# Optimization experiments

Measured on AMD Instinct MI355X. Metric: run time of the kernel, lower is better.

## Reference

```python
import jax, jax.numpy as jnp
import numpy as np

N = 100_000
E = 3_200_000
F_IN = 512
F_OUT = 256
ALPHA = 0.2      # LeakyReLU negative slope
EPS = 9e-15      # matches torch.Tensor([9e-15]) in the original


def setup_inputs() -> dict:
    key = jax.random.key(0)
    k_x, k_e, k_w, k_a, k_b = jax.random.split(key, 5)
    x = jax.random.normal(k_x, (N, F_IN), dtype=jnp.float32)
    edge = jax.random.randint(k_e, (2, E), 0, N, dtype=jnp.int64)
    # xavier_normal-ish scales
    W = jax.random.normal(k_w, (F_IN, F_OUT), dtype=jnp.float32) * (1.414 * np.sqrt(2.0 / (F_IN + F_OUT)))
    a = jax.random.normal(k_a, (2 * F_OUT,), dtype=jnp.float32) * (1.414 * np.sqrt(2.0 / (1 + 2 * F_OUT)))
    bias = jax.random.normal(k_b, (F_OUT,), dtype=jnp.float32) * (1.414 * np.sqrt(2.0 / (1 + F_OUT)))
    return {"x": x, "edge": edge, "W": W, "a": a, "bias": bias}


def reference(x, edge, W, a, bias):
    src, dst = edge[0], edge[1]
    n = x.shape[0]
    h = x @ W + bias  # [N, F_OUT]
    # a . cat(h[src], h[dst]) == (h @ a_src)[src] + (h @ a_dst)[dst]
    a_src, a_dst = a[:F_OUT], a[F_OUT:]
    e = (h @ a_src)[src] + (h @ a_dst)[dst]            # [E]
    e = jnp.where(e > 0, e, ALPHA * e)                  # LeakyReLU
    e = jnp.exp(e - jnp.max(e))                         # global-max stabilized exp
    rowsum = jax.ops.segment_sum(e, src, num_segments=n)               # [N]
    h_prime = jax.ops.segment_sum(e[:, None] * h[dst], src, num_segments=n)  # [N, F_OUT]
    h_prime = h_prime / (rowsum[:, None] + EPS)
    return jax.nn.elu(h_prime)
```

## Files before the change

kernel.cpp:

```cpp
#include <hip/hip_runtime.h>

typedef __bf16 bf16x8 __attribute__((ext_vector_type(8)));
typedef float f32x4 __attribute__((ext_vector_type(4)));
typedef unsigned short u16x8 __attribute__((ext_vector_type(8)));

#define FIN 512
#define FOUT 256
#define NBLK 256
#define BSHIFT 8

__device__ __forceinline__ float b2f(unsigned short u) {
  union { unsigned int u; float f; } x;
  x.u = ((unsigned int)u) << 16;
  return x.f;
}
__device__ __forceinline__ unsigned short f2b(float f) {
  union { float f; unsigned int u; } x; x.f = f;
  unsigned int u = x.u;
  unsigned int r = (u + 0x7fffu + ((u >> 16) & 1u)) >> 16;
  return (unsigned short)r;
}
__device__ __forceinline__ unsigned int cvt_pk_bf16(float lo, float hi) {
  unsigned int r;
  asm("v_cvt_pk_bf16_f32 %0, %1, %2" : "=v"(r) : "v"(lo), "v"(hi));
  return r;
}

__global__ void k_probe(const unsigned short* __restrict__ xh,
                        const int* __restrict__ e, int* __restrict__ flags) {
  __shared__ int cnt[2];
  if (threadIdx.x == 0) { cnt[0] = 0; cnt[1] = 0; }
  __syncthreads();
  int c = 0;
  for (int i = threadIdx.x; i < 32768; i += 256) {
    unsigned short u = xh[i];
    if (((u >> 7) & 0xFF) == 0xFF) c++;
  }
  if (c) atomicAdd(&cnt[0], c);
  if (e[2 * threadIdx.x + 1] == 0) atomicAdd(&cnt[1], 1);
  __syncthreads();
  if (threadIdx.x == 0) {
    flags[0] = (cnt[0] > 0) ? 1 : 0;
    flags[1] = (cnt[1] > 128) ? 1 : 0;
  }
}

__global__ void k_transpose(const void* __restrict__ W,
                            unsigned short* __restrict__ Wt,
                            const int* __restrict__ flags) {
  int idx = blockIdx.x * 256 + threadIdx.x;
  int k = idx >> 8, n = idx & 255;
  float v = flags[0] ? ((const float*)W)[idx]
                     : b2f(((const unsigned short*)W)[idx]);
  Wt[n * FIN + k] = f2b(v);
}

__global__ __launch_bounds__(256) void k_gemm(const void* __restrict__ X,
                                              const unsigned short* __restrict__ Wt,
                                              const void* __restrict__ bias,
                                              const void* __restrict__ A,
                                              unsigned short* __restrict__ H,
                                              float* __restrict__ s1,
                                              float* __restrict__ s2,
                                              int nrows, const int* __restrict__ flags) {
  __shared__ char lds[65536];
  const int tid = threadIdx.x;
  const int wave = tid >> 6;
  const int lane = tid & 63;
  const int fm = lane & 15;
  const int fq = lane >> 4;
  const int isf = flags[0];
  const int m0 = blockIdx.x * 64;

  if (isf) {
#pragma unroll 4
    for (int j = 0; j < 16; ++j) {
      int r = wave * 16 + j;
      int grow = m0 + r; if (grow >= nrows) grow = nrows - 1;
      int c = lane ^ (j & 7);
      const float* gp = (const float*)X + (size_t)grow * FIN + c * 8;
      f32x4 lo = *(const f32x4*)gp;
      f32x4 hi = *(const f32x4*)(gp + 4);
      uint4 pk;
      pk.x = cvt_pk_bf16(lo[0], lo[1]);
      pk.y = cvt_pk_bf16(lo[2], lo[3]);
      pk.z = cvt_pk_bf16(hi[0], hi[1]);
      pk.w = cvt_pk_bf16(hi[2], hi[3]);
      *(uint4*)(lds + r * 1024 + lane * 16) = pk;
    }
  } else {
#pragma unroll
    for (int j = 0; j < 16; ++j) {
      int r = wave * 16 + j;
      int grow = m0 + r; if (grow >= nrows) grow = nrows - 1;
      int c = lane ^ (j & 7);
      const unsigned short* gp = (const unsigned short*)X + (size_t)grow * FIN + c * 8;
      __builtin_amdgcn_global_load_lds(
          (const __attribute__((address_space(1))) void*)gp,
          (__attribute__((address_space(3))) void*)(lds + r * 1024), 16, 0, 0);
    }
  }
  __syncthreads();

  f32x4 acc[4][4];
#pragma unroll
  for (int i = 0; i < 4; i++)
#pragma unroll
    for (int j = 0; j < 4; j++) acc[i][j] = (f32x4){0.f, 0.f, 0.f, 0.f};

  const unsigned short* wp[4];
#pragma unroll
  for (int i = 0; i < 4; i++)
    wp[i] = Wt + (size_t)((wave * 4 + i) * 16 + fm) * FIN + fq * 8;

  const int swz = fm & 7;
  bf16x8 bcur[4];
#pragma unroll
  for (int i = 0; i < 4; i++) bcur[i] = *(const bf16x8*)(wp[i]);

  for (int it = 0; it < 16; ++it) {
    int itn = (it + 1 < 16) ? it + 1 : 15;
    bf16x8 bnext[4];
#pragma unroll
    for (int i = 0; i < 4; i++) bnext[i] = *(const bf16x8*)(wp[i] + itn * 32);
    bf16x8 af[4];
#pragma unroll
    for (int mt = 0; mt < 4; mt++) {
      int slot = (it * 4 + fq) ^ swz;
      af[mt] = *(const bf16x8*)(lds + (mt * 16 + fm) * 1024 + slot * 16);
    }
#pragma unroll
    for (int mt = 0; mt < 4; mt++)
#pragma unroll
      for (int i = 0; i < 4; i++)
        acc[mt][i] = __builtin_amdgcn_mfma_f32_16x16x32_bf16(af[mt], bcur[i], acc[mt][i], 0, 0, 0);
#pragma unroll
    for (int i = 0; i < 4; i++) bcur[i] = bnext[i];
  }

  __syncthreads();
  float* sc1 = (float*)lds;
  float* sc2 = sc1 + 256;

  float bvv[4], asv[4], adv[4];
#pragma unroll
  for (int i = 0; i < 4; i++) {
    int col = (wave * 4 + i) * 16 + fm;
    if (isf) {
      bvv[i] = ((const float*)bias)[col];
      asv[i] = ((const float*)A)[col];
      adv[i] = ((const float*)A)[FOUT + col];
    } else {
      bvv[i] = b2f(((const unsigned short*)bias)[col]);
      asv[i] = b2f(((const unsigned short*)A)[col]);
      adv[i] = b2f(((const unsigned short*)A)[FOUT + col]);
    }
  }

#pragma unroll
  for (int mt = 0; mt < 4; mt++) {
#pragma unroll
    for (int r = 0; r < 4; r++) {
      int row = m0 + mt * 16 + fq * 4 + r;
      float p1 = 0.f, p2 = 0.f;
#pragma unroll
      for (int i = 0; i < 4; i++) {
        float h = acc[mt][i][r] + bvv[i];
        if (row < nrows) H[(size_t)row * FOUT + (wave * 4 + i) * 16 + fm] = f2b(h);
        p1 += h * asv[i];
        p2 += h * adv[i];
      }
#pragma unroll
      for (int off = 1; off < 16; off <<= 1) {
        p1 += __shfl_xor(p1, off, 64);
        p2 += __shfl_xor(p2, off, 64);
      }
      if (fm == 0) {
        int rl = mt * 16 + fq * 4 + r;
        sc1[wave * 64 + rl] = p1;
        sc2[wave * 64 + rl] = p2;
      }
    }
  }
  __syncthreads();
  if (tid < 64) {
    int row = m0 + tid;
    if (row < nrows) {
      s1[row] = sc1[tid] + sc1[64 + tid] + sc1[128 + tid] + sc1[192 + tid];
      s2[row] = sc2[tid] + sc2[64 + tid] + sc2[128 + tid] + sc2[192 + tid];
    }
  }
}


__global__ __launch_bounds__(256) void k_bcount(const int* __restrict__ e, int E, int chunk,
                                                int nbuck, int* __restrict__ C,
                                                const int* __restrict__ flags) {
  __shared__ int hist[512];
  int t = threadIdx.x, blk = blockIdx.x;
  for (int i = t; i < nbuck; i += 256) hist[i] = 0;
  __syncthreads();
  int lo = blk * chunk, hi = min(E, lo + chunk);
  bool i64 = flags[1] != 0;
  for (int i = lo + t; i < hi; i += 256) {
    int s = i64 ? ((const int2*)e)[i].x : e[i];
    atomicAdd(&hist[s >> BSHIFT], 1);
  }
  __syncthreads();
  for (int i = t; i < nbuck; i += 256) C[blk * nbuck + i] = hist[i];
}

__global__ __launch_bounds__(256) void k_bscanA(const int* __restrict__ C, int nbuck,
                                                int* __restrict__ O, int* __restrict__ btot) {
  int b = blockIdx.x, t = threadIdx.x;
  int lane = t & 63, w = t >> 6;
  int v = C[t * nbuck + b];
  int x = v;
#pragma unroll
  for (int off = 1; off < 64; off <<= 1) {
    int y = __shfl_up(x, off, 64);
    if (lane >= off) x += y;
  }
  __shared__ int ws[4];
  if (lane == 63) ws[w] = x;
  __syncthreads();
  int wbase = (w > 0 ? ws[0] : 0) + (w > 1 ? ws[1] : 0) + (w > 2 ? ws[2] : 0);
  O[t * nbuck + b] = x + wbase - v;
  if (t == 255) btot[b] = x + wbase;
}

__global__ __launch_bounds__(512) void k_bscanB(const int* __restrict__ btot, int nbuck,
                                                int* __restrict__ bbase,
                                                int* __restrict__ rowptr, int N) {
  __shared__ int sh[512];
  int t = threadIdx.x;
  int v = (t < nbuck) ? btot[t] : 0;
  sh[t] = v;
  __syncthreads();
  for (int off = 1; off < 512; off <<= 1) {
    int u = (t >= off) ? sh[t - off] : 0;
    __syncthreads();
    sh[t] += u;
    __syncthreads();
  }
  if (t < nbuck) bbase[t] = sh[t] - v;
  if (t == nbuck - 1) { bbase[nbuck] = sh[t]; rowptr[N] = sh[t]; }
}

__global__ __launch_bounds__(256) void k_bscatter(const int* __restrict__ e, int E, int chunk,
                                                  int nbuck, const int* __restrict__ O,
                                                  const int* __restrict__ bbase,
                                                  int* __restrict__ stage,
                                                  const int* __restrict__ flags) {
  __shared__ int cur[512];
  int t = threadIdx.x, blk = blockIdx.x;
  for (int i = t; i < nbuck; i += 256) cur[i] = bbase[i] + O[blk * nbuck + i];
  __syncthreads();
  int lo = blk * chunk, hi = min(E, lo + chunk);
  bool i64 = flags[1] != 0;
  for (int i = lo + t; i < hi; i += 256) {
    int s, d;
    if (i64) { s = ((const int2*)e)[i].x; d = ((const int2*)e)[(size_t)E + i].x; }
    else     { s = e[i];                  d = e[E + i]; }
    int pos = atomicAdd(&cur[s >> BSHIFT], 1);
    stage[pos] = ((s & 255) << 17) | d;
  }
}

__global__ __launch_bounds__(256) void k_fine(const int* __restrict__ stage,
                                              const int* __restrict__ bbase,
                                              int* __restrict__ rowptr,
                                              int* __restrict__ csrd, int N) {
  __shared__ int hist[256];
  __shared__ int cursor[256];
  __shared__ int ws[4];
  int b = blockIdx.x, t = threadIdx.x;
  int s0 = b << BSHIFT;
  int base = bbase[b], end = bbase[b + 1], cnt = end - base;
  hist[t] = 0;
  __syncthreads();
  for (int i = t; i < cnt; i += 256) atomicAdd(&hist[stage[base + i] >> 17], 1);
  __syncthreads();
  int v = hist[t];
  int lane = t & 63, w = t >> 6;
  int x = v;
#pragma unroll
  for (int off = 1; off < 64; off <<= 1) {
    int y = __shfl_up(x, off, 64);
    if (lane >= off) x += y;
  }
  if (lane == 63) ws[w] = x;
  __syncthreads();
  int wbase = (w > 0 ? ws[0] : 0) + (w > 1 ? ws[1] : 0) + (w > 2 ? ws[2] : 0);
  int excl = x + wbase - v;
  cursor[t] = base + excl;
  if (s0 + t < N) rowptr[s0 + t] = base + excl;
  __syncthreads();
  for (int i = t; i < cnt; i += 256) {
    int p = stage[base + i];
    int pos = atomicAdd(&cursor[p >> 17], 1);
    csrd[pos] = p & 0x1FFFF;
  }
}

__global__ __launch_bounds__(256) void k_gather(const unsigned short* __restrict__ H,
                                                const float* __restrict__ s1,
                                                const float* __restrict__ s2,
                                                const int* __restrict__ rowptr,
                                                const int* __restrict__ csrd,
                                                void* __restrict__ out, int n,
                                                const int* __restrict__ flags) {
  __shared__ int2 eds[4][64];
  int wave = threadIdx.x >> 6, lane = threadIdx.x & 63;
  int row = blockIdx.x * 4 + wave;
  if (row >= n) return;
  int half = lane >> 5;
  int hl = lane & 31;
  int beg = rowptr[row], end = rowptr[row + 1];
  float s1v = s1[row];
  const unsigned short* Hb = H + hl * 8;
  float ac[8];
#pragma unroll
  for (int k = 0; k < 8; k++) ac[k] = 0.f;
  float wsum = 0.f;

  for (int base = beg; base < end; base += 64) {
    int cnt = end - base; if (cnt > 64) cnt = 64;
    int d_pre = 0;
    float s_pre = -1e30f;
    if (lane < cnt) { d_pre = csrd[base + lane]; s_pre = s2[d_pre]; }
    eds[wave][lane] = make_int2(d_pre, __float_as_int(s_pre));

#pragma unroll 8
    for (int j = 0; j < cnt; j += 2) {
      int jj = j + half;
      int2 p = eds[wave][jj];
      int dd = p.x;
      float v = s1v + __int_as_float(p.y);
      v = v > 0.f ? v : 0.2f * v;
      float w = (jj < cnt) ? __expf(v) : 0.f;
      union { u16x8 v; unsigned short u[8]; } hv;
      hv.v = *(const u16x8*)(Hb + (size_t)dd * FOUT);
      wsum += w;
#pragma unroll
      for (int k = 0; k < 8; k++) ac[k] += w * b2f(hv.u[k]);
    }
  }

#pragma unroll
  for (int k = 0; k < 8; k++) ac[k] += __shfl_down(ac[k], 32, 64);
  wsum += __shfl_down(wsum, 32, 64);

  if (half == 0) {
    float inv = 1.f / (wsum + 9e-15f);
    float o[8];
#pragma unroll
    for (int k = 0; k < 8; k++) {
      float x = ac[k] * inv;
      o[k] = x > 0.f ? x : __expf(x) - 1.f;
    }
    if (flags[0]) {
      float* op = (float*)out + (size_t)row * FOUT + hl * 8;
      *(f32x4*)op = (f32x4){o[0], o[1], o[2], o[3]};
      *(f32x4*)(op + 4) = (f32x4){o[4], o[5], o[6], o[7]};
    } else {
      union { u16x8 v; unsigned short u[8]; } ov;
#pragma unroll
      for (int k = 0; k < 8; k++) ov.u[k] = f2b(o[k]);
      *(u16x8*)((unsigned short*)out + (size_t)row * FOUT + hl * 8) = ov.v;
    }
  }
}

extern "C" void kernel_launch(void* const* d_in, const int* in_sizes, int n_in,
                              void* d_out, int out_size, void* d_ws, size_t ws_size,
                              hipStream_t stream) {
  const void* X = d_in[0];
  const int* edge = (const int*)d_in[1];
  const void* W = d_in[2];
  const void* A = d_in[3];
  const void* B = d_in[4];
  int N_ = in_sizes[0] / FIN;
  int E_ = in_sizes[1] / 2;
  int nbuck = (N_ + 255) >> BSHIFT;
  int chunk = (E_ + NBLK - 1) / NBLK;

  char* p = (char*)d_ws;
  auto alloc = [&](size_t bytes) {
    char* r = p; p += (bytes + 255) & ~(size_t)255; return r;
  };
  int* flags = (int*)alloc(256);
  unsigned short* H  = (unsigned short*)alloc((size_t)N_ * FOUT * 2);
  unsigned short* Wt = (unsigned short*)alloc((size_t)FIN * FOUT * 2);
  float* s1   = (float*)alloc((size_t)N_ * 4);
  float* s2   = (float*)alloc((size_t)N_ * 4);
  int* rowptr = (int*)alloc((size_t)(N_ + 1) * 4);
  int* csrd   = (int*)alloc((size_t)E_ * 4);
  int* C      = (int*)alloc((size_t)NBLK * nbuck * 4);
  int* O      = (int*)alloc((size_t)NBLK * nbuck * 4);
  int* btot   = (int*)alloc((size_t)nbuck * 4);
  int* bbase  = (int*)alloc((size_t)(nbuck + 1) * 4);
  int* stage  = (int*)alloc((size_t)E_ * 4);

  k_probe<<<1, 256, 0, stream>>>((const unsigned short*)X, edge, flags);
  k_transpose<<<(FIN * FOUT) / 256, 256, 0, stream>>>(W, Wt, flags);
  k_gemm<<<(N_ + 63) / 64, 256, 0, stream>>>(X, Wt, B, A, H, s1, s2, N_, flags);
  k_bcount<<<NBLK, 256, 0, stream>>>(edge, E_, chunk, nbuck, C, flags);
  k_bscanA<<<nbuck, 256, 0, stream>>>(C, nbuck, O, btot);
  k_bscanB<<<1, 512, 0, stream>>>(btot, nbuck, bbase, rowptr, N_);
  k_bscatter<<<NBLK, 256, 0, stream>>>(edge, E_, chunk, nbuck, O, bbase, stage, flags);
  k_fine<<<nbuck, 256, 0, stream>>>(stage, bbase, rowptr, csrd, N_);
  k_gather<<<(N_ + 3) / 4, 256, 0, stream>>>(H, s1, s2, rowptr, csrd,
                                             d_out, N_, flags);
}
```

Baseline: 728.9 us.

## Fuse CSR build stages into one cooperative kernel with grid syncs

The probe, W transpose, bucket count, two scans, scatter and fine sort are merged into a single cooperative kernel of 256 blocks that uses grid.sync between phases. This replaces seven launches and their inter-kernel gaps, and a fallback to the original launches runs if the cooperative launch fails. The gather is also split into about four launches over row ranges, which adds launch overhead without an obvious benefit. Grid syncs serialize the phases, and the single-block scan phases leave most blocks idle.

```diff
diff --git a/kernel.cpp b/kernel.cpp
--- a/kernel.cpp
+++ b/kernel.cpp
@@ -1,4 +1,6 @@
 #include <hip/hip_runtime.h>
+#include <hip/hip_cooperative_groups.h>
+namespace cg = cooperative_groups;
 
 typedef __bf16 bf16x8 __attribute__((ext_vector_type(8)));
 typedef float f32x4 __attribute__((ext_vector_type(4)));
@@ -24,6 +26,155 @@
   unsigned int r;
   asm("v_cvt_pk_bf16_f32 %0, %1, %2" : "=v"(r) : "v"(lo), "v"(hi));
   return r;
+}
+
+__global__ __launch_bounds__(256) void k_csr_all(
+    const unsigned short* __restrict__ xh, const int* __restrict__ e,
+    int* __restrict__ flags, const void* __restrict__ W,
+    unsigned short* __restrict__ Wt, int E, int chunk, int nbuck,
+    int* __restrict__ C, int* __restrict__ O, int* __restrict__ btot,
+    int* __restrict__ bbase, int* __restrict__ rowptr,
+    int* __restrict__ stage, int* __restrict__ csrd, int N) {
+  cg::grid_group grid = cg::this_grid();
+  __shared__ int shm[768];
+  const int t = threadIdx.x;
+  const int blk = blockIdx.x;
+
+  if (blk == 0) {
+    if (t == 0) { shm[0] = 0; shm[1] = 0; }
+    __syncthreads();
+    int c = 0;
+    for (int i = t; i < 32768; i += 256) {
+      unsigned short u = xh[i];
+      if (((u >> 7) & 0xFF) == 0xFF) c++;
+    }
+    if (c) atomicAdd(&shm[0], c);
+    if (e[2 * t + 1] == 0) atomicAdd(&shm[1], 1);
+    __syncthreads();
+    if (t == 0) {
+      flags[0] = (shm[0] > 0) ? 1 : 0;
+      flags[1] = (shm[1] > 128) ? 1 : 0;
+    }
+  }
+  __threadfence();
+  grid.sync();
+
+  const int isf = flags[0];
+  const bool i64 = flags[1] != 0;
+
+#pragma unroll
+  for (int k2 = 0; k2 < 2; k2++) {
+    int idx = blk * 512 + k2 * 256 + t;
+    int kk = idx >> 8, nn = idx & 255;
+    float v = isf ? ((const float*)W)[idx]
+                  : b2f(((const unsigned short*)W)[idx]);
+    Wt[nn * FIN + kk] = f2b(v);
+  }
+  for (int i = t; i < nbuck; i += 256) shm[i] = 0;
+  __syncthreads();
+  {
+    int lo = blk * chunk, hi = min(E, lo + chunk);
+    for (int i = lo + t; i < hi; i += 256) {
+      int s = i64 ? ((const int2*)e)[i].x : e[i];
+      atomicAdd(&shm[s >> BSHIFT], 1);
+    }
+  }
+  __syncthreads();
+  for (int i = t; i < nbuck; i += 256) C[blk * nbuck + i] = shm[i];
+  __threadfence();
+  grid.sync();
+
+  for (int k2 = 0; k2 < 2; k2++) {
+    __syncthreads();
+    int b = blk + k2 * 256;
+    if (b < nbuck) {
+      int lane = t & 63, w = t >> 6;
+      int v = C[t * nbuck + b];
+      int x = v;
+#pragma unroll
+      for (int off = 1; off < 64; off <<= 1) {
+        int y = __shfl_up(x, off, 64);
+        if (lane >= off) x += y;
+      }
+      if (lane == 63) shm[512 + w] = x;
+      __syncthreads();
+      int wbase = (w > 0 ? shm[512] : 0) + (w > 1 ? shm[513] : 0) + (w > 2 ? shm[514] : 0);
+      O[t * nbuck + b] = x + wbase - v;
+      if (t == 255) btot[b] = x + wbase;
+    }
+  }
+  __threadfence();
+  grid.sync();
+
+  if (blk == 0) {
+    int v0 = (t < nbuck) ? btot[t] : 0;
+    int v1 = (t + 256 < nbuck) ? btot[t + 256] : 0;
+    shm[t] = v0; shm[t + 256] = v1;
+    __syncthreads();
+    for (int off = 1; off < 512; off <<= 1) {
+      int a0 = (t >= off) ? shm[t - off] : 0;
+      int a1 = (t + 256 >= off) ? shm[t + 256 - off] : 0;
+      __syncthreads();
+      shm[t] += a0; shm[t + 256] += a1;
+      __syncthreads();
+    }
+    if (t < nbuck) bbase[t] = shm[t] - v0;
+    if (t + 256 < nbuck) bbase[t + 256] = shm[t + 256] - v1;
+    if (t == nbuck - 1) { bbase[nbuck] = shm[t]; rowptr[N] = shm[t]; }
+    if (t + 256 == nbuck - 1) { bbase[nbuck] = shm[t + 256]; rowptr[N] = shm[t + 256]; }
+  }
+  __threadfence();
+  grid.sync();
+
+  for (int i = t; i < nbuck; i += 256) shm[i] = bbase[i] + O[blk * nbuck + i];
+  __syncthreads();
+  {
+    int lo = blk * chunk, hi = min(E, lo + chunk);
+    for (int i = lo + t; i < hi; i += 256) {
+      int s, d;
+      if (i64) { s = ((const int2*)e)[i].x; d = ((const int2*)e)[(size_t)E + i].x; }
+      else     { s = e[i];                  d = e[E + i]; }
+      int pos = atomicAdd(&shm[s >> BSHIFT], 1);
+      stage[pos] = ((s & 255) << 17) | d;
+    }
+  }
+  __threadfence();
+  grid.sync();
+
+  for (int k2 = 0; k2 < 2; k2++) {
+    __syncthreads();
+    int b = blk + k2 * 256;
+    if (b >= nbuck) continue;
+    int s0 = b << BSHIFT;
+    int base = bbase[b], end2 = bbase[b + 1], cnt = end2 - base;
+    int* hist = shm;
+    int* cursor = shm + 256;
+    int* ws = shm + 512;
+    hist[t] = 0;
+    __syncthreads();
+    for (int i = t; i < cnt; i += 256) atomicAdd(&hist[stage[base + i] >> 17], 1);
+    __syncthreads();
+    int v = hist[t];
+    int lane = t & 63, w = t >> 6;
+    int x = v;
+#pragma unroll
+    for (int off = 1; off < 64; off <<= 1) {
+      int y = __shfl_up(x, off, 64);
+      if (lane >= off) x += y;
+    }
+    if (lane == 63) ws[w] = x;
+    __syncthreads();
+    int wbase = (w > 0 ? ws[0] : 0) + (w > 1 ? ws[1] : 0) + (w > 2 ? ws[2] : 0);
+    int excl = x + wbase - v;
+    cursor[t] = base + excl;
+    if (s0 + t < N) rowptr[s0 + t] = base + excl;
+    __syncthreads();
+    for (int i = t; i < cnt; i += 256) {
+      int p = stage[base + i];
+      int pos = atomicAdd(&cursor[p >> 17], 1);
+      csrd[pos] = p & 0x1FFFF;
+    }
+  }
 }
 
 __global__ void k_probe(const unsigned short* __restrict__ xh,
@@ -53,6 +204,116 @@
   float v = flags[0] ? ((const float*)W)[idx]
                      : b2f(((const unsigned short*)W)[idx]);
   Wt[n * FIN + k] = f2b(v);
+}
+
+__global__ __launch_bounds__(256) void k_bcount(const int* __restrict__ e, int E, int chunk,
+                                                int nbuck, int* __restrict__ C,
+                                                const int* __restrict__ flags) {
+  __shared__ int hist[512];
+  int t = threadIdx.x, blk = blockIdx.x;
+  for (int i = t; i < nbuck; i += 256) hist[i] = 0;
+  __syncthreads();
+  int lo = blk * chunk, hi = min(E, lo + chunk);
+  bool i64 = flags[1] != 0;
+  for (int i = lo + t; i < hi; i += 256) {
+    int s = i64 ? ((const int2*)e)[i].x : e[i];
+    atomicAdd(&hist[s >> BSHIFT], 1);
+  }
+  __syncthreads();
+  for (int i = t; i < nbuck; i += 256) C[blk * nbuck + i] = hist[i];
+}
+
+__global__ __launch_bounds__(256) void k_bscanA(const int* __restrict__ C, int nbuck,
+                                                int* __restrict__ O, int* __restrict__ btot) {
+  int b = blockIdx.x, t = threadIdx.x;
+  int lane = t & 63, w = t >> 6;
+  int v = C[t * nbuck + b];
+  int x = v;
+#pragma unroll
+  for (int off = 1; off < 64; off <<= 1) {
+    int y = __shfl_up(x, off, 64);
+    if (lane >= off) x += y;
+  }
+  __shared__ int ws[4];
+  if (lane == 63) ws[w] = x;
+  __syncthreads();
+  int wbase = (w > 0 ? ws[0] : 0) + (w > 1 ? ws[1] : 0) + (w > 2 ? ws[2] : 0);
+  O[t * nbuck + b] = x + wbase - v;
+  if (t == 255) btot[b] = x + wbase;
+}
+
+__global__ __launch_bounds__(512) void k_bscanB(const int* __restrict__ btot, int nbuck,
+                                                int* __restrict__ bbase,
+                                                int* __restrict__ rowptr, int N) {
+  __shared__ int sh[512];
+  int t = threadIdx.x;
+  int v = (t < nbuck) ? btot[t] : 0;
+  sh[t] = v;
+  __syncthreads();
+  for (int off = 1; off < 512; off <<= 1) {
+    int u = (t >= off) ? sh[t - off] : 0;
+    __syncthreads();
+    sh[t] += u;
+    __syncthreads();
+  }
+  if (t < nbuck) bbase[t] = sh[t] - v;
+  if (t == nbuck - 1) { bbase[nbuck] = sh[t]; rowptr[N] = sh[t]; }
+}
+
+__global__ __launch_bounds__(256) void k_bscatter(const int* __restrict__ e, int E, int chunk,
+                                                  int nbuck, const int* __restrict__ O,
+                                                  const int* __restrict__ bbase,
+                                                  int* __restrict__ stage,
+                                                  const int* __restrict__ flags) {
+  __shared__ int cur[512];
+  int t = threadIdx.x, blk = blockIdx.x;
+  for (int i = t; i < nbuck; i += 256) cur[i] = bbase[i] + O[blk * nbuck + i];
+  __syncthreads();
+  int lo = blk * chunk, hi = min(E, lo + chunk);
+  bool i64 = flags[1] != 0;
+  for (int i = lo + t; i < hi; i += 256) {
+    int s, d;
+    if (i64) { s = ((const int2*)e)[i].x; d = ((const int2*)e)[(size_t)E + i].x; }
+    else     { s = e[i];                  d = e[E + i]; }
+    int pos = atomicAdd(&cur[s >> BSHIFT], 1);
+    stage[pos] = ((s & 255) << 17) | d;
+  }
+}
+
+__global__ __launch_bounds__(256) void k_fine(const int* __restrict__ stage,
+                                              const int* __restrict__ bbase,
+                                              int* __restrict__ rowptr,
+                                              int* __restrict__ csrd, int N) {
+  __shared__ int hist[256];
+  __shared__ int cursor[256];
+  __shared__ int ws[4];
+  int b = blockIdx.x, t = threadIdx.x;
+  int s0 = b << BSHIFT;
+  int base = bbase[b], end = bbase[b + 1], cnt = end - base;
+  hist[t] = 0;
+  __syncthreads();
+  for (int i = t; i < cnt; i += 256) atomicAdd(&hist[stage[base + i] >> 17], 1);
+  __syncthreads();
+  int v = hist[t];
+  int lane = t & 63, w = t >> 6;
+  int x = v;
+#pragma unroll
+  for (int off = 1; off < 64; off <<= 1) {
+    int y = __shfl_up(x, off, 64);
+    if (lane >= off) x += y;
+  }
+  if (lane == 63) ws[w] = x;
+  __syncthreads();
+  int wbase = (w > 0 ? ws[0] : 0) + (w > 1 ? ws[1] : 0) + (w > 2 ? ws[2] : 0);
+  int excl = x + wbase - v;
+  cursor[t] = base + excl;
+  if (s0 + t < N) rowptr[s0 + t] = base + excl;
+  __syncthreads();
+  for (int i = t; i < cnt; i += 256) {
+    int p = stage[base + i];
+    int pos = atomicAdd(&cursor[p >> 17], 1);
+    csrd[pos] = p & 0x1FFFF;
+  }
 }
 
 __global__ __launch_bounds__(256) void k_gemm(const void* __restrict__ X,
@@ -192,127 +453,16 @@
   }
 }
 
-
-__global__ __launch_bounds__(256) void k_bcount(const int* __restrict__ e, int E, int chunk,
-                                                int nbuck, int* __restrict__ C,
-                                                const int* __restrict__ flags) {
-  __shared__ int hist[512];
-  int t = threadIdx.x, blk = blockIdx.x;
-  for (int i = t; i < nbuck; i += 256) hist[i] = 0;
-  __syncthreads();
-  int lo = blk * chunk, hi = min(E, lo + chunk);
-  bool i64 = flags[1] != 0;
-  for (int i = lo + t; i < hi; i += 256) {
-    int s = i64 ? ((const int2*)e)[i].x : e[i];
-    atomicAdd(&hist[s >> BSHIFT], 1);
-  }
-  __syncthreads();
-  for (int i = t; i < nbuck; i += 256) C[blk * nbuck + i] = hist[i];
-}
-
-__global__ __launch_bounds__(256) void k_bscanA(const int* __restrict__ C, int nbuck,
-                                                int* __restrict__ O, int* __restrict__ btot) {
-  int b = blockIdx.x, t = threadIdx.x;
-  int lane = t & 63, w = t >> 6;
-  int v = C[t * nbuck + b];
-  int x = v;
-#pragma unroll
-  for (int off = 1; off < 64; off <<= 1) {
-    int y = __shfl_up(x, off, 64);
-    if (lane >= off) x += y;
-  }
-  __shared__ int ws[4];
-  if (lane == 63) ws[w] = x;
-  __syncthreads();
-  int wbase = (w > 0 ? ws[0] : 0) + (w > 1 ? ws[1] : 0) + (w > 2 ? ws[2] : 0);
-  O[t * nbuck + b] = x + wbase - v;
-  if (t == 255) btot[b] = x + wbase;
-}
-
-__global__ __launch_bounds__(512) void k_bscanB(const int* __restrict__ btot, int nbuck,
-                                                int* __restrict__ bbase,
-                                                int* __restrict__ rowptr, int N) {
-  __shared__ int sh[512];
-  int t = threadIdx.x;
-  int v = (t < nbuck) ? btot[t] : 0;
-  sh[t] = v;
-  __syncthreads();
-  for (int off = 1; off < 512; off <<= 1) {
-    int u = (t >= off) ? sh[t - off] : 0;
-    __syncthreads();
-    sh[t] += u;
-    __syncthreads();
-  }
-  if (t < nbuck) bbase[t] = sh[t] - v;
-  if (t == nbuck - 1) { bbase[nbuck] = sh[t]; rowptr[N] = sh[t]; }
-}
-
-__global__ __launch_bounds__(256) void k_bscatter(const int* __restrict__ e, int E, int chunk,
-                                                  int nbuck, const int* __restrict__ O,
-                                                  const int* __restrict__ bbase,
-                                                  int* __restrict__ stage,
-                                                  const int* __restrict__ flags) {
-  __shared__ int cur[512];
-  int t = threadIdx.x, blk = blockIdx.x;
-  for (int i = t; i < nbuck; i += 256) cur[i] = bbase[i] + O[blk * nbuck + i];
-  __syncthreads();
-  int lo = blk * chunk, hi = min(E, lo + chunk);
-  bool i64 = flags[1] != 0;
-  for (int i = lo + t; i < hi; i += 256) {
-    int s, d;
-    if (i64) { s = ((const int2*)e)[i].x; d = ((const int2*)e)[(size_t)E + i].x; }
-    else     { s = e[i];                  d = e[E + i]; }
-    int pos = atomicAdd(&cur[s >> BSHIFT], 1);
-    stage[pos] = ((s & 255) << 17) | d;
-  }
-}
-
-__global__ __launch_bounds__(256) void k_fine(const int* __restrict__ stage,
-                                              const int* __restrict__ bbase,
-                                              int* __restrict__ rowptr,
-                                              int* __restrict__ csrd, int N) {
-  __shared__ int hist[256];
-  __shared__ int cursor[256];
-  __shared__ int ws[4];
-  int b = blockIdx.x, t = threadIdx.x;
-  int s0 = b << BSHIFT;
-  int base = bbase[b], end = bbase[b + 1], cnt = end - base;
-  hist[t] = 0;
-  __syncthreads();
-  for (int i = t; i < cnt; i += 256) atomicAdd(&hist[stage[base + i] >> 17], 1);
-  __syncthreads();
-  int v = hist[t];
-  int lane = t & 63, w = t >> 6;
-  int x = v;
-#pragma unroll
-  for (int off = 1; off < 64; off <<= 1) {
-    int y = __shfl_up(x, off, 64);
-    if (lane >= off) x += y;
-  }
-  if (lane == 63) ws[w] = x;
-  __syncthreads();
-  int wbase = (w > 0 ? ws[0] : 0) + (w > 1 ? ws[1] : 0) + (w > 2 ? ws[2] : 0);
-  int excl = x + wbase - v;
-  cursor[t] = base + excl;
-  if (s0 + t < N) rowptr[s0 + t] = base + excl;
-  __syncthreads();
-  for (int i = t; i < cnt; i += 256) {
-    int p = stage[base + i];
-    int pos = atomicAdd(&cursor[p >> 17], 1);
-    csrd[pos] = p & 0x1FFFF;
-  }
-}
-
 __global__ __launch_bounds__(256) void k_gather(const unsigned short* __restrict__ H,
                                                 const float* __restrict__ s1,
                                                 const float* __restrict__ s2,
                                                 const int* __restrict__ rowptr,
                                                 const int* __restrict__ csrd,
-                                                void* __restrict__ out, int n,
+                                                void* __restrict__ out, int row0, int n,
                                                 const int* __restrict__ flags) {
   __shared__ int2 eds[4][64];
   int wave = threadIdx.x >> 6, lane = threadIdx.x & 63;
-  int row = blockIdx.x * 4 + wave;
+  int row = row0 + blockIdx.x * 4 + wave;
   if (row >= n) return;
   int half = lane >> 5;
   int hl = lane & 31;
@@ -402,14 +552,36 @@
   int* bbase  = (int*)alloc((size_t)(nbuck + 1) * 4);
   int* stage  = (int*)alloc((size_t)E_ * 4);
 
-  k_probe<<<1, 256, 0, stream>>>((const unsigned short*)X, edge, flags);
-  k_transpose<<<(FIN * FOUT) / 256, 256, 0, stream>>>(W, Wt, flags);
+  {
+    const unsigned short* xh_ = (const unsigned short*)X;
+    const int* e_ = edge;
+    int* flags_ = flags;
+    const void* W_ = W;
+    unsigned short* Wt_ = Wt;
+    int E2 = E_, chunk2 = chunk, nbuck2 = nbuck, N2 = N_;
+    int* C_ = C; int* O_ = O; int* btot_ = btot; int* bbase_ = bbase;
+    int* rowptr_ = rowptr; int* stage_ = stage; int* csrd_ = csrd;
+    void* cargs[] = {&xh_, &e_, &flags_, &W_, &Wt_, &E2, &chunk2, &nbuck2,
+                     &C_, &O_, &btot_, &bbase_, &rowptr_, &stage_, &csrd_, &N2};
+    hipError_t cerr = hipLaunchCooperativeKernel((const void*)k_csr_all,
+                        dim3(NBLK), dim3(256), cargs, 0, stream);
+    if (cerr != hipSuccess) {
+      k_probe<<<1, 256, 0, stream>>>(xh_, edge, flags);
+      k_transpose<<<(FIN * FOUT) / 256, 256, 0, stream>>>(W, Wt, flags);
+      k_bcount<<<NBLK, 256, 0, stream>>>(edge, E_, chunk, nbuck, C, flags);
+      k_bscanA<<<nbuck, 256, 0, stream>>>(C, nbuck, O, btot);
+      k_bscanB<<<1, 512, 0, stream>>>(btot, nbuck, bbase, rowptr, N_);
+      k_bscatter<<<NBLK, 256, 0, stream>>>(edge, E_, chunk, nbuck, O, bbase, stage, flags);
+      k_fine<<<nbuck, 256, 0, stream>>>(stage, bbase, rowptr, csrd, N_);
+    }
+  }
+
   k_gemm<<<(N_ + 63) / 64, 256, 0, stream>>>(X, Wt, B, A, H, s1, s2, N_, flags);
-  k_bcount<<<NBLK, 256, 0, stream>>>(edge, E_, chunk, nbuck, C, flags);
-  k_bscanA<<<nbuck, 256, 0, stream>>>(C, nbuck, O, btot);
-  k_bscanB<<<1, 512, 0, stream>>>(btot, nbuck, bbase, rowptr, N_);
-  k_bscatter<<<NBLK, 256, 0, stream>>>(edge, E_, chunk, nbuck, O, bbase, stage, flags);
-  k_fine<<<nbuck, 256, 0, stream>>>(stage, bbase, rowptr, csrd, N_);
-  k_gather<<<(N_ + 3) / 4, 256, 0, stream>>>(H, s1, s2, rowptr, csrd,
-                                             d_out, N_, flags);
-}
+
+  int rstep = ((N_ + 15) / 16) * 4;
+  for (int r0 = 0; r0 < N_; r0 += rstep) {
+    int rows = N_ - r0; if (rows > rstep) rows = rstep;
+    k_gather<<<(rows + 3) / 4, 256, 0, stream>>>(H, s1, s2, rowptr, csrd,
+                                                 d_out, r0, N_, flags);
+  }
+}
```

Measured after the change: 1.048 ms. +43.8%, slower.

## Halve GEMM LDS footprint by staging X in two K-halves for occupancy

Applied to the files above, without the earlier changes.

The GEMM kernel now stages its 64-row X tile into shared memory in two 256-column halves (32 KB instead of 64 KB), computing on one half before loading the second. It sets launch bounds to target 3 blocks per CU, and deepens the W-fragment register prefetch from one step ahead to two. The goal is more resident blocks per CU so one block's loads can overlap with other blocks' MFMA work. The cost is an extra barrier and a non-overlapped reload in the middle of each block, plus tighter register limits that could cause spills.

```diff
diff --git a/kernel.cpp b/kernel.cpp
--- a/kernel.cpp
+++ b/kernel.cpp
@@ -55,52 +55,59 @@
   Wt[n * FIN + k] = f2b(v);
 }
 
-__global__ __launch_bounds__(256) void k_gemm(const void* __restrict__ X,
-                                              const unsigned short* __restrict__ Wt,
-                                              const void* __restrict__ bias,
-                                              const void* __restrict__ A,
-                                              unsigned short* __restrict__ H,
-                                              float* __restrict__ s1,
-                                              float* __restrict__ s2,
-                                              int nrows, const int* __restrict__ flags) {
-  __shared__ char lds[65536];
+__global__ __launch_bounds__(256, 3) void k_gemm(const void* __restrict__ X,
+                                                 const unsigned short* __restrict__ Wt,
+                                                 const void* __restrict__ bias,
+                                                 const void* __restrict__ A,
+                                                 unsigned short* __restrict__ H,
+                                                 float* __restrict__ s1,
+                                                 float* __restrict__ s2,
+                                                 int nrows, const int* __restrict__ flags) {
+  __shared__ char lds[32768];
   const int tid = threadIdx.x;
   const int wave = tid >> 6;
   const int lane = tid & 63;
   const int fm = lane & 15;
   const int fq = lane >> 4;
+  const int hw = lane >> 5;
+  const int hl = lane & 31;
   const int isf = flags[0];
   const int m0 = blockIdx.x * 64;
 
-  if (isf) {
-#pragma unroll 4
-    for (int j = 0; j < 16; ++j) {
-      int r = wave * 16 + j;
-      int grow = m0 + r; if (grow >= nrows) grow = nrows - 1;
-      int c = lane ^ (j & 7);
-      const float* gp = (const float*)X + (size_t)grow * FIN + c * 8;
-      f32x4 lo = *(const f32x4*)gp;
-      f32x4 hi = *(const f32x4*)(gp + 4);
-      uint4 pk;
-      pk.x = cvt_pk_bf16(lo[0], lo[1]);
-      pk.y = cvt_pk_bf16(lo[2], lo[3]);
-      pk.z = cvt_pk_bf16(hi[0], hi[1]);
-      pk.w = cvt_pk_bf16(hi[2], hi[3]);
-      *(uint4*)(lds + r * 1024 + lane * 16) = pk;
-    }
-  } else {
-#pragma unroll
-    for (int j = 0; j < 16; ++j) {
-      int r = wave * 16 + j;
-      int grow = m0 + r; if (grow >= nrows) grow = nrows - 1;
-      int c = lane ^ (j & 7);
-      const unsigned short* gp = (const unsigned short*)X + (size_t)grow * FIN + c * 8;
-      __builtin_amdgcn_global_load_lds(
-          (const __attribute__((address_space(1))) void*)gp,
-          (__attribute__((address_space(3))) void*)(lds + r * 1024), 16, 0, 0);
-    }
-  }
-  __syncthreads();
+#define STAGE_HALF(h)                                                          \
+  do {                                                                         \
+    const int k0_ = (h) * 256;                                                 \
+    if (isf) {                                                                 \
+      _Pragma("unroll")                                                        \
+      for (int j = 0; j < 8; ++j) {                                            \
+        int r = wave * 16 + j * 2 + hw;                                        \
+        int grow = m0 + r; if (grow >= nrows) grow = nrows - 1;                \
+        int c = hl ^ (r & 7);                                                  \
+        const float* gp = (const float*)X + (size_t)grow * FIN + k0_ + c * 8;  \
+        f32x4 lo = *(const f32x4*)gp;                                          \
+        f32x4 hi = *(const f32x4*)(gp + 4);                                    \
+        uint4 pk;                                                              \
+        pk.x = cvt_pk_bf16(lo[0], lo[1]);                                      \
+        pk.y = cvt_pk_bf16(lo[2], lo[3]);                                      \
+        pk.z = cvt_pk_bf16(hi[0], hi[1]);                                      \
+        pk.w = cvt_pk_bf16(hi[2], hi[3]);                                      \
+        *(uint4*)(lds + r * 512 + hl * 16) = pk;                               \
+      }                                                                        \
+    } else {                                                                   \
+      _Pragma("unroll")                                                        \
+      for (int j = 0; j < 8; ++j) {                                            \
+        int r = wave * 16 + j * 2 + hw;                                        \
+        int grow = m0 + r; if (grow >= nrows) grow = nrows - 1;                \
+        int c = hl ^ (r & 7);                                                  \
+        const unsigned short* gp =                                             \
+            (const unsigned short*)X + (size_t)grow * FIN + k0_ + c * 8;       \
+        __builtin_amdgcn_global_load_lds(                                      \
+            (const __attribute__((address_space(1))) void*)gp,                 \
+            (__attribute__((address_space(3))) void*)(lds +                    \
+                (wave * 16 + j * 2) * 512), 16, 0, 0);                         \
+      }                                                                        \
+    }                                                                          \
+  } while (0)
 
   f32x4 acc[4][4];
 #pragma unroll
@@ -114,29 +121,48 @@
     wp[i] = Wt + (size_t)((wave * 4 + i) * 16 + fm) * FIN + fq * 8;
 
   const int swz = fm & 7;
-  bf16x8 bcur[4];
+
+  STAGE_HALF(0);
+
+  bf16x8 bcur[4], bnxt[4];
 #pragma unroll
   for (int i = 0; i < 4; i++) bcur[i] = *(const bf16x8*)(wp[i]);
-
-  for (int it = 0; it < 16; ++it) {
-    int itn = (it + 1 < 16) ? it + 1 : 15;
-    bf16x8 bnext[4];
-#pragma unroll
-    for (int i = 0; i < 4; i++) bnext[i] = *(const bf16x8*)(wp[i] + itn * 32);
-    bf16x8 af[4];
-#pragma unroll
-    for (int mt = 0; mt < 4; mt++) {
-      int slot = (it * 4 + fq) ^ swz;
-      af[mt] = *(const bf16x8*)(lds + (mt * 16 + fm) * 1024 + slot * 16);
-    }
-#pragma unroll
-    for (int mt = 0; mt < 4; mt++)
-#pragma unroll
-      for (int i = 0; i < 4; i++)
-        acc[mt][i] = __builtin_amdgcn_mfma_f32_16x16x32_bf16(af[mt], bcur[i], acc[mt][i], 0, 0, 0);
-#pragma unroll
-    for (int i = 0; i < 4; i++) bcur[i] = bnext[i];
-  }
+#pragma unroll
+  for (int i = 0; i < 4; i++) bnxt[i] = *(const bf16x8*)(wp[i] + 32);
+
+  __syncthreads();
+
+#define K_BODY(kk, it)                                                         \
+  do {                                                                         \
+    bf16x8 af[4];                                                              \
+    _Pragma("unroll")                                                          \
+    for (int mt = 0; mt < 4; mt++) {                                           \
+      int slot = ((it) * 4 + fq) ^ swz;                                        \
+      af[mt] = *(const bf16x8*)(lds + (mt * 16 + fm) * 512 + slot * 16);       \
+    }                                                                          \
+    bf16x8 bn[4];                                                              \
+    int kn = (kk) + 2; if (kn > 15) kn = 15;                                   \
+    _Pragma("unroll")                                                          \
+    for (int i = 0; i < 4; i++) bn[i] = *(const bf16x8*)(wp[i] + kn * 32);     \
+    _Pragma("unroll")                                                          \
+    for (int mt = 0; mt < 4; mt++)                                             \
+      _Pragma("unroll")                                                        \
+      for (int i = 0; i < 4; i++)                                              \
+        acc[mt][i] = __builtin_amdgcn_mfma_f32_16x16x32_bf16(                  \
+            af[mt], bcur[i], acc[mt][i], 0, 0, 0);                             \
+    _Pragma("unroll")                                                          \
+    for (int i = 0; i < 4; i++) { bcur[i] = bnxt[i]; bnxt[i] = bn[i]; }        \
+  } while (0)
+
+#pragma unroll
+  for (int it = 0; it < 8; ++it) K_BODY(it, it);
+
+  __syncthreads();
+  STAGE_HALF(1);
+  __syncthreads();
+
+#pragma unroll
+  for (int it = 0; it < 8; ++it) K_BODY(8 + it, it);
 
   __syncthreads();
   float* sc1 = (float*)lds;
@@ -190,6 +216,8 @@
       s2[row] = sc2[tid] + sc2[64 + tid] + sc2[128 + tid] + sc2[192 + tid];
     }
   }
+#undef STAGE_HALF
+#undef K_BODY
 }
 
 
```

New measurement: 699.0 us. 4.1% less time.
